# Kernel optimization log

Measured on AMD Instinct MI355X. Metric: run time of the kernel, lower is better.

## Reference

```python
import jax, jax.numpy as jnp
import numpy as np

N_MI, N_DI = 100000, 50000   # node counts
E, L = 500000, 200000        # message edges, supervision (label) edges
F_MI, F_DI, H = 256, 128, 128


def setup_inputs() -> dict:
    key = jax.random.key(0)
    ks = iter(jax.random.split(key, 40))

    def nrm(shape, scale):
        return jax.random.normal(next(ks), shape, jnp.float32) * scale

    inp = {
        'x_mi': jax.random.normal(next(ks), (N_MI, F_MI), jnp.float32),
        'x_di': jax.random.normal(next(ks), (N_DI, F_DI), jnp.float32),
        'W_mi': nrm((H, F_MI), 1.0 / np.sqrt(F_MI)),
        'b_mi': jnp.zeros((H,), jnp.float32),
        'W_di': nrm((H, F_DI), 1.0 / np.sqrt(F_DI)),
        'b_di': jnp.zeros((H,), jnp.float32),
        'emb_mi': nrm((N_MI, H), 1.0),
        'emb_di': nrm((N_DI, H), 1.0),
    }
    # SAGEConv weights per layer per relation (md: miRNA->disease, dm: reverse)
    dims = [(H, 256), (256, 128), (128, 64)]
    for i, (ci, co) in enumerate(dims, 1):
        for rel in ('md', 'dm'):
            inp[f'Wl{i}_{rel}'] = nrm((co, ci), 1.0 / np.sqrt(ci))  # neighbor lin (with bias)
            inp[f'bl{i}_{rel}'] = jnp.zeros((co,), jnp.float32)
            inp[f'Wr{i}_{rel}'] = nrm((co, ci), 1.0 / np.sqrt(ci))  # root lin (no bias)
    inp['edge_src'] = jax.random.randint(next(ks), (E,), 0, N_MI)
    inp['edge_dst'] = jax.random.randint(next(ks), (E,), 0, N_DI)
    inp['label_src'] = jax.random.randint(next(ks), (L,), 0, N_MI)
    inp['label_dst'] = jax.random.randint(next(ks), (L,), 0, N_DI)
    return inp


def _sage(x_src, x_dst, src, dst, n_dst, Wl, bl, Wr):
    # PyG SAGEConv (mean aggr): out = lin_l(mean_neighbors) + lin_r(x_dst)
    agg = jax.ops.segment_sum(x_src[src], dst, num_segments=n_dst)
    deg = jax.ops.segment_sum(jnp.ones_like(dst, dtype=x_src.dtype), dst, num_segments=n_dst)
    mean = agg / jnp.maximum(deg, 1.0)[:, None]
    return mean @ Wl.T + bl + x_dst @ Wr.T


def reference(x_mi, x_di, W_mi, b_mi, W_di, b_di, emb_mi, emb_di,
              Wl1_md, bl1_md, Wr1_md, Wl1_dm, bl1_dm, Wr1_dm,
              Wl2_md, bl2_md, Wr2_md, Wl2_dm, bl2_dm, Wr2_dm,
              Wl3_md, bl3_md, Wr3_md, Wl3_dm, bl3_dm, Wr3_dm,
              edge_src, edge_dst, label_src, label_dst):
    # node_id == arange(num_nodes), so the embedding lookup is the full table
    h_mi = x_mi @ W_mi.T + b_mi + emb_mi
    h_di = x_di @ W_di.T + b_di + emb_di
    layers = [((Wl1_md, bl1_md, Wr1_md), (Wl1_dm, bl1_dm, Wr1_dm)),
              ((Wl2_md, bl2_md, Wr2_md), (Wl2_dm, bl2_dm, Wr2_dm)),
              ((Wl3_md, bl3_md, Wr3_md), (Wl3_dm, bl3_dm, Wr3_dm))]
    for li, (pmd, pdm) in enumerate(layers):
        new_di = _sage(h_mi, h_di, edge_src, edge_dst, N_DI, *pmd)  # miRNA -> disease
        new_mi = _sage(h_di, h_mi, edge_dst, edge_src, N_MI, *pdm)  # disease -> miRNA (reverse)
        if li < 2:
            new_mi, new_di = jax.nn.relu(new_mi), jax.nn.relu(new_di)
        h_mi, h_di = new_mi, new_di
    # classifier: dot product on supervision edges -> [L]
    return (h_mi[label_src] * h_di[label_dst]).sum(axis=-1)
```

## Files before the change

### kernel.cpp

```cpp
#include <hip/hip_runtime.h>

#define N_MI 100000
#define N_DI 50000
#define MI_P 100352
#define DI_P 50176

#define SCAN_CHUNK 2048
#define NB_DI ((N_DI + SCAN_CHUNK - 1) / SCAN_CHUNK)
#define NB_MI ((N_MI + SCAN_CHUNK - 1) / SCAN_CHUNK)

typedef _Float16 half8  __attribute__((ext_vector_type(8)));
typedef _Float16 half4  __attribute__((ext_vector_type(4)));
typedef float    floatx4 __attribute__((ext_vector_type(4)));

__global__ void count_kernel(const int* __restrict__ src, const int* __restrict__ dst,
                             int* deg_mi, int* deg_di, int E) {
    int i = blockIdx.x * blockDim.x + threadIdx.x;
    if (i < E) {
        atomicAdd(&deg_mi[src[i]], 1);
        atomicAdd(&deg_di[dst[i]], 1);
    }
}

__global__ __launch_bounds__(256) void scan_part_kernel(const int* __restrict__ deg_di,
                                                        const int* __restrict__ deg_mi,
                                                        int* __restrict__ row_di,
                                                        int* __restrict__ row_mi,
                                                        int* __restrict__ bsum) {
    const int* deg; int* row; int n; int* bs;
    if (blockIdx.y == 0) { deg = deg_di; row = row_di; n = N_DI; bs = bsum; }
    else                 { deg = deg_mi; row = row_mi; n = N_MI; bs = bsum + 64; }
    int nb = (n + SCAN_CHUNK - 1) / SCAN_CHUNK;
    if ((int)blockIdx.x >= nb) return;
    int t = threadIdx.x;
    int base = blockIdx.x * SCAN_CHUNK + t * 8;
    int v[8]; int s = 0;
    #pragma unroll
    for (int e = 0; e < 8; ++e) {
        int i = base + e;
        v[e] = (i < n) ? deg[i] : 0;
        s += v[e];
    }
    int lane = t & 63, w = t >> 6;
    int x = s;
    #pragma unroll
    for (int off = 1; off < 64; off <<= 1) {
        int y = __shfl_up(x, off, 64);
        if (lane >= off) x += y;
    }
    __shared__ int wsum[4];
    if (lane == 63) wsum[w] = x;
    __syncthreads();
    int woff = 0;
    #pragma unroll
    for (int i = 0; i < 3; ++i) if (i < w) woff += wsum[i];
    int run = woff + x - s;
    #pragma unroll
    for (int e = 0; e < 8; ++e) {
        int i = base + e;
        if (i < n) row[i] = run;
        run += v[e];
    }
    if (t == 255) bs[blockIdx.x] = woff + x;
}

__global__ void scan_sums_kernel(int* __restrict__ bsum, int* __restrict__ row_di,
                                 int* __restrict__ row_mi) {
    int w = threadIdx.x >> 6, lane = threadIdx.x & 63;
    int nb = (w == 0) ? NB_DI : NB_MI;
    int* bs = bsum + w * 64;
    int v = (lane < nb) ? bs[lane] : 0;
    int x = v;
    #pragma unroll
    for (int off = 1; off < 64; off <<= 1) {
        int y = __shfl_up(x, off, 64);
        if (lane >= off) x += y;
    }
    if (lane < nb) bs[lane] = x - v;
    if (lane == nb - 1) {
        if (w == 0) row_di[N_DI] = x;
        else        row_mi[N_MI] = x;
    }
}

__global__ __launch_bounds__(256) void scan_add_kernel(const int* __restrict__ bsum,
                                                       int* __restrict__ row_di,
                                                       int* __restrict__ row_mi) {
    int* row; int n; const int* bs;
    if (blockIdx.y == 0) { row = row_di; n = N_DI; bs = bsum; }
    else                 { row = row_mi; n = N_MI; bs = bsum + 64; }
    int nb = (n + SCAN_CHUNK - 1) / SCAN_CHUNK;
    int b = blockIdx.x;
    if (b >= nb || b == 0) return;
    int off = bs[b];
    int base = b * SCAN_CHUNK + threadIdx.x;
    #pragma unroll
    for (int e = 0; e < 8; ++e) {
        int i = base + e * 256;
        if (i < n) row[i] += off;
    }
}

__global__ void fill_kernel(const int* __restrict__ src, const int* __restrict__ dst,
                            const int* __restrict__ row_mi, const int* __restrict__ row_di,
                            int* cur_mi, int* cur_di, int* csr_mi, int* csr_di, int E) {
    int i = blockIdx.x * blockDim.x + threadIdx.x;
    if (i >= E) return;
    int s = src[i], d = dst[i];
    int p = atomicAdd(&cur_di[d], 1);
    csr_di[row_di[d] + p] = s;
    int q = atomicAdd(&cur_mi[s], 1);
    csr_mi[row_mi[s] + q] = d;
}


struct CvtW {
    const float* s[14];
    _Float16* d[14];
    int K[14];
    int KI[14];
    int nch[14];
};

__global__ void cvtw_kernel(CvtW a) {
    int arr = blockIdx.y;
    int c = blockIdx.x * blockDim.x + threadIdx.x;
    if (c >= a.nch[arr]) return;
    int K = a.K[arr], KI = a.KI[arr];
    int lane = c & 63;
    int j = (c >> 6) & 3;
    int rest = c >> 8;
    int k = rest % KI;
    int p = rest / KI;
    int row = p * 64 + j * 16 + (lane & 15);
    int kcol = k * 32 + (lane >> 4) * 8;
    const float* s = a.s[arr] + (long)row * K + kcol;
    float4 u = *(const float4*)s;
    float4 v = *(const float4*)(s + 4);
    half8 h = {(_Float16)u.x, (_Float16)u.y, (_Float16)u.z, (_Float16)u.w,
               (_Float16)v.x, (_Float16)v.y, (_Float16)v.z, (_Float16)v.w};
    *(half8*)(a.d[arr] + (long)c * 8) = h;
}

template<int K>
__global__ __launch_bounds__(256) void cvt_frag(const float* __restrict__ in,
                                                _Float16* __restrict__ out, int M) {
    constexpr int KI = K / 32;
    constexpr int CPR = K / 8;
    __shared__ _Float16 lds[64 * (K + 8)];
    const int tile = blockIdx.x;
    const int tid = threadIdx.x;
    #pragma unroll
    for (int it = 0; it < KI; ++it) {
        int c = tid + it * 256;
        int r = c / CPR, col = c % CPR;
        int row = tile * 64 + r;
        if (row >= M) row = M - 1;
        const float* g = in + (long)row * K + col * 8;
        float4 u = *(const float4*)g;
        float4 v = *(const float4*)(g + 4);
        half8 h = {(_Float16)u.x, (_Float16)u.y, (_Float16)u.z, (_Float16)u.w,
                   (_Float16)v.x, (_Float16)v.y, (_Float16)v.z, (_Float16)v.w};
        *(half8*)&lds[r * (K + 8) + col * 8] = h;
    }
    __syncthreads();
    #pragma unroll
    for (int it = 0; it < KI; ++it) {
        int c = tid + it * 256;
        int lane = c & 63, i = (c >> 6) & 3, k = c >> 8;
        half8 h = *(const half8*)&lds[(i * 16 + (lane & 15)) * (K + 8) + k * 32 + (lane >> 4) * 8];
        *(half8*)(out + ((long)tile * 8 * K + c) * 8) = h;
    }
}

template<int K>
__global__ __launch_bounds__(256) void repack(const _Float16* __restrict__ in,
                                              _Float16* __restrict__ out) {
    constexpr int KI = K / 32;
    constexpr int CPR = K / 8;
    __shared__ _Float16 lds[64 * (K + 8)];
    const int tile = blockIdx.x;
    const int tid = threadIdx.x;
    #pragma unroll
    for (int it = 0; it < KI; ++it) {
        int c = tid + it * 256;
        int r = c / CPR, col = c % CPR;
        half8 h = *(const half8*)(in + (long)tile * 64 * K + c * 8);
        *(half8*)&lds[r * (K + 8) + col * 8] = h;
    }
    __syncthreads();
    #pragma unroll
    for (int it = 0; it < KI; ++it) {
        int c = tid + it * 256;
        int lane = c & 63, i = (c >> 6) & 3, k = c >> 8;
        half8 h = *(const half8*)&lds[(i * 16 + (lane & 15)) * (K + 8) + k * 32 + (lane >> 4) * 8];
        *(half8*)(out + ((long)tile * 8 * K + c) * 8) = h;
    }
}

template<int DIN>
__global__ __launch_bounds__(256) void agg2_kernel(const _Float16* __restrict__ hsrc,
                                                   const int* __restrict__ row,
                                                   const int* __restrict__ csr,
                                                   _Float16* __restrict__ outf, int n) {
    constexpr int LPR = DIN / 8;
    constexpr int GR  = 64 / LPR;
    constexpr int KI  = DIN / 32;
    int node = blockIdx.x * 4 + (threadIdx.x >> 6);
    if (node >= n) return;
    int lane = threadIdx.x & 63;
    int g = lane / LPR, c = lane % LPR;
    int beg = row[node], end = row[node + 1];
    float acc[8] = {};
    #pragma unroll 2
    for (int j = beg + g; j < end; j += GR) {
        half8 v = *(const half8*)(hsrc + (long)csr[j] * DIN + c * 8);
        #pragma unroll
        for (int e = 0; e < 8; ++e) acc[e] += (float)v[e];
    }
    float inv = 1.f / (float)max(end - beg, 1);
    half8 o;
    #pragma unroll
    for (int e = 0; e < 8; ++e) {
        float s = acc[e];
        s += __shfl_down(s, 32);
        if (GR == 4) s += __shfl_down(s, 16);
        o[e] = (_Float16)(s * inv);
    }
    if (g == 0) {
        int mt = node >> 6, ii = (node >> 4) & 3, lrm = node & 15;
        long off = (((long)mt * KI + (c >> 2)) * 4 + ii) * 512 + (lrm + 16 * (c & 3)) * 8;
        *(half8*)(outf + off) = o;
    }
}

template<int KI, bool DUAL>
__global__ __launch_bounds__(256, 3) void hgemm_f(
    const _Float16* __restrict__ A1f, const _Float16* __restrict__ W1f,
    const _Float16* __restrict__ A2f, const _Float16* __restrict__ W2f,
    const float* __restrict__ bias, const float* __restrict__ Cadd,
    _Float16* __restrict__ C, int M, int N, int relu)
{
    const int wave = threadIdx.x >> 6, lane = threadIdx.x & 63;
    const int quad = lane >> 4, lr = lane & 15;
    const int mt = blockIdx.x * 4 + wave;
    const int p = blockIdx.y;
    const long abase = ((long)mt * KI * 4) * 512 + lane * 8;
    const long wbase = ((long)p  * KI * 4) * 512 + lane * 8;

    floatx4 acc[4][4] = {};

    #pragma unroll
    for (int pass = 0; pass < (DUAL ? 2 : 1); ++pass) {
        const _Float16* A = pass ? A2f : A1f;
        const _Float16* W = pass ? W2f : W1f;
        #pragma unroll
        for (int k = 0; k < KI; ++k) {
            half8 af[4], bf[4];
            #pragma unroll
            for (int i = 0; i < 4; ++i)
                af[i] = *(const half8*)(A + abase + (k * 4 + i) * 512);
            #pragma unroll
            for (int j = 0; j < 4; ++j)
                bf[j] = *(const half8*)(W + wbase + (k * 4 + j) * 512);
            #pragma unroll
            for (int i = 0; i < 4; ++i)
                #pragma unroll
                for (int j = 0; j < 4; ++j)
                    acc[i][j] = __builtin_amdgcn_mfma_f32_16x16x32_f16(af[i], bf[j], acc[i][j], 0, 0, 0);
        }
    }

    const int m0 = mt * 64, n0 = p * 64;
    #pragma unroll
    for (int i = 0; i < 4; ++i) {
        int mb = m0 + i * 16 + quad * 4;
        #pragma unroll
        for (int j = 0; j < 4; ++j) {
            int n = n0 + j * 16 + lr;
            float bn = bias[n];
            #pragma unroll
            for (int r = 0; r < 4; ++r) {
                int m = mb + r;
                if (m < M) {
                    float v = acc[i][j][r] + bn;
                    if (Cadd) v += Cadd[(long)m * N + n];
                    if (relu) v = fmaxf(v, 0.f);
                    C[(long)m * N + n] = (_Float16)v;
                }
            }
        }
    }
}

__global__ void classify_kernel(const _Float16* __restrict__ hmi, const _Float16* __restrict__ hdi,
                                const int* __restrict__ ls, const int* __restrict__ ld,
                                float* __restrict__ out, int L) {
    long idx = (long)blockIdx.x * blockDim.x + threadIdx.x;
    int e = (int)(idx >> 4), q = (int)(idx & 15);
    if (e >= L) return;
    const half4* ra = (const half4*)(hmi + (long)ls[e] * 64);
    const half4* rb = (const half4*)(hdi + (long)ld[e] * 64);
    half4 a = ra[q], b = rb[q];
    float s = (float)a.x * (float)b.x + (float)a.y * (float)b.y +
              (float)a.z * (float)b.z + (float)a.w * (float)b.w;
    #pragma unroll
    for (int off = 8; off >= 1; off >>= 1) s += __shfl_down(s, off, 16);
    if (q == 0) out[e] = s;
}

extern "C" void kernel_launch(void* const* d_in, const int* in_sizes, int n_in,
                              void* d_out, int out_size, void* d_ws, size_t ws_size,
                              hipStream_t stream) {
    const float* x_mi   = (const float*)d_in[0];
    const float* x_di   = (const float*)d_in[1];
    const float* W_mi   = (const float*)d_in[2];
    const float* b_mi   = (const float*)d_in[3];
    const float* W_di   = (const float*)d_in[4];
    const float* b_di   = (const float*)d_in[5];
    const float* emb_mi = (const float*)d_in[6];
    const float* emb_di = (const float*)d_in[7];
    const float* Wl1_md = (const float*)d_in[8];
    const float* bl1_md = (const float*)d_in[9];
    const float* Wr1_md = (const float*)d_in[10];
    const float* Wl1_dm = (const float*)d_in[11];
    const float* bl1_dm = (const float*)d_in[12];
    const float* Wr1_dm = (const float*)d_in[13];
    const float* Wl2_md = (const float*)d_in[14];
    const float* bl2_md = (const float*)d_in[15];
    const float* Wr2_md = (const float*)d_in[16];
    const float* Wl2_dm = (const float*)d_in[17];
    const float* bl2_dm = (const float*)d_in[18];
    const float* Wr2_dm = (const float*)d_in[19];
    const float* Wl3_md = (const float*)d_in[20];
    const float* bl3_md = (const float*)d_in[21];
    const float* Wr3_md = (const float*)d_in[22];
    const float* Wl3_dm = (const float*)d_in[23];
    const float* bl3_dm = (const float*)d_in[24];
    const float* Wr3_dm = (const float*)d_in[25];
    const int* edge_src  = (const int*)d_in[26];
    const int* edge_dst  = (const int*)d_in[27];
    const int* label_src = (const int*)d_in[28];
    const int* label_dst = (const int*)d_in[29];
    const int E = in_sizes[26];
    const int L = in_sizes[28];
    float* out = (float*)d_out;

    _Float16* hp = (_Float16*)d_ws;
    _Float16* wWmi  = hp; hp += 128 * 256;
    _Float16* wWdi  = hp; hp += 128 * 128;
    _Float16* wl1md = hp; hp += 256 * 128;
    _Float16* wr1md = hp; hp += 256 * 128;
    _Float16* wl1dm = hp; hp += 256 * 128;
    _Float16* wr1dm = hp; hp += 256 * 128;
    _Float16* wl2md = hp; hp += 128 * 256;
    _Float16* wr2md = hp; hp += 128 * 256;
    _Float16* wl2dm = hp; hp += 128 * 256;
    _Float16* wr2dm = hp; hp += 128 * 256;
    _Float16* wl3md = hp; hp += 64 * 128;
    _Float16* wr3md = hp; hp += 64 * 128;
    _Float16* wl3dm = hp; hp += 64 * 128;
    _Float16* wr3dm = hp; hp += 64 * 128;
    _Float16* h_mi0 = hp; hp += (long)MI_P * 256;
    _Float16* h_mi1 = hp; hp += (long)MI_P * 256;
    _Float16* h_di0 = hp; hp += (long)DI_P * 256;
    _Float16* h_di1 = hp; hp += (long)DI_P * 256;
    _Float16* hf_mi = hp; hp += (long)MI_P * 256;
    _Float16* hf_di = hp; hp += (long)DI_P * 256;
    _Float16* agghf = hp; hp += (long)MI_P * 256;

    int* ip = (int*)hp;
    int* deg_di = ip;  ip += N_DI;
    int* deg_mi = ip;  ip += N_MI;
    int* cur_di = ip;  ip += N_DI;
    int* cur_mi = ip;  ip += N_MI;
    int* row_di = ip;  ip += N_DI + 1;
    int* row_mi = ip;  ip += N_MI + 1;
    int* csr_di = ip;  ip += E;
    int* csr_mi = ip;  ip += E;
    int* bsum   = ip;  ip += 128;

    hipMemsetAsync(deg_di, 0, (size_t)(2 * (N_DI + N_MI)) * sizeof(int), stream);
    int eb = (E + 255) / 256;
    count_kernel<<<eb, 256, 0, stream>>>(edge_src, edge_dst, deg_mi, deg_di, E);
    scan_part_kernel<<<dim3(NB_MI, 2), 256, 0, stream>>>(deg_di, deg_mi, row_di, row_mi, bsum);
    scan_sums_kernel<<<1, 128, 0, stream>>>(bsum, row_di, row_mi);
    scan_add_kernel<<<dim3(NB_MI, 2), 256, 0, stream>>>(bsum, row_di, row_mi);
    fill_kernel<<<eb, 256, 0, stream>>>(edge_src, edge_dst, row_mi, row_di,
                                        cur_mi, cur_di, csr_mi, csr_di, E);

    CvtW cw;
    const float* srcs[14] = {W_mi, W_di, Wl1_md, Wr1_md, Wl1_dm, Wr1_dm,
                             Wl2_md, Wr2_md, Wl2_dm, Wr2_dm, Wl3_md, Wr3_md, Wl3_dm, Wr3_dm};
    _Float16* dsts[14] = {wWmi, wWdi, wl1md, wr1md, wl1dm, wr1dm,
                          wl2md, wr2md, wl2dm, wr2dm, wl3md, wr3md, wl3dm, wr3dm};
    int Ks[14]  = {256, 128, 128, 128, 128, 128, 256, 256, 256, 256, 128, 128, 128, 128};
    int Ns[14]  = {128, 128, 256, 256, 256, 256, 128, 128, 128, 128, 64, 64, 64, 64};
    for (int i = 0; i < 14; ++i) {
        cw.s[i] = srcs[i]; cw.d[i] = dsts[i];
        cw.K[i] = Ks[i]; cw.KI[i] = Ks[i] / 32;
        cw.nch[i] = Ns[i] * Ks[i] / 8;
    }
    cvtw_kernel<<<dim3(16, 14), 256, 0, stream>>>(cw);

    cvt_frag<256><<<MI_P / 64, 256, 0, stream>>>(x_mi, hf_mi, N_MI);
    cvt_frag<128><<<DI_P / 64, 256, 0, stream>>>(x_di, hf_di, N_DI);

    hgemm_f<8, false><<<dim3(MI_P / 256, 2), 256, 0, stream>>>(
        hf_mi, wWmi, nullptr, nullptr, b_mi, emb_mi, h_mi0, N_MI, 128, 0);
    hgemm_f<4, false><<<dim3(DI_P / 256, 2), 256, 0, stream>>>(
        hf_di, wWdi, nullptr, nullptr, b_di, emb_di, h_di0, N_DI, 128, 0);

    repack<128><<<MI_P / 64, 256, 0, stream>>>(h_mi0, hf_mi);
    repack<128><<<DI_P / 64, 256, 0, stream>>>(h_di0, hf_di);
    agg2_kernel<128><<<(N_DI + 3) / 4, 256, 0, stream>>>(h_mi0, row_di, csr_di, agghf, N_DI);
    hgemm_f<4, true><<<dim3(DI_P / 256, 4), 256, 0, stream>>>(
        agghf, wl1md, hf_di, wr1md, bl1_md, nullptr, h_di1, N_DI, 256, 1);
    agg2_kernel<128><<<(N_MI + 3) / 4, 256, 0, stream>>>(h_di0, row_mi, csr_mi, agghf, N_MI);
    hgemm_f<4, true><<<dim3(MI_P / 256, 4), 256, 0, stream>>>(
        agghf, wl1dm, hf_mi, wr1dm, bl1_dm, nullptr, h_mi1, N_MI, 256, 1);

    repack<256><<<MI_P / 64, 256, 0, stream>>>(h_mi1, hf_mi);
    repack<256><<<DI_P / 64, 256, 0, stream>>>(h_di1, hf_di);
    agg2_kernel<256><<<(N_DI + 3) / 4, 256, 0, stream>>>(h_mi1, row_di, csr_di, agghf, N_DI);
    hgemm_f<8, true><<<dim3(DI_P / 256, 2), 256, 0, stream>>>(
        agghf, wl2md, hf_di, wr2md, bl2_md, nullptr, h_di0, N_DI, 128, 1);
    agg2_kernel<256><<<(N_MI + 3) / 4, 256, 0, stream>>>(h_di1, row_mi, csr_mi, agghf, N_MI);
    hgemm_f<8, true><<<dim3(MI_P / 256, 2), 256, 0, stream>>>(
        agghf, wl2dm, hf_mi, wr2dm, bl2_dm, nullptr, h_mi0, N_MI, 128, 1);

    repack<128><<<MI_P / 64, 256, 0, stream>>>(h_mi0, hf_mi);
    repack<128><<<DI_P / 64, 256, 0, stream>>>(h_di0, hf_di);
    agg2_kernel<128><<<(N_DI + 3) / 4, 256, 0, stream>>>(h_mi0, row_di, csr_di, agghf, N_DI);
    hgemm_f<4, true><<<dim3(DI_P / 256, 1), 256, 0, stream>>>(
        agghf, wl3md, hf_di, wr3md, bl3_md, nullptr, h_di1, N_DI, 64, 0);
    agg2_kernel<128><<<(N_MI + 3) / 4, 256, 0, stream>>>(h_di0, row_mi, csr_mi, agghf, N_MI);
    hgemm_f<4, true><<<dim3(MI_P / 256, 1), 256, 0, stream>>>(
        agghf, wl3dm, hf_mi, wr3dm, bl3_dm, nullptr, h_mi1, N_MI, 64, 0);

    classify_kernel<<<((long)L * 16 + 255) / 256, 256, 0, stream>>>(
        h_mi1, h_di1, label_src, label_dst, out, L);
}
```

Baseline: 892.8 us.

## Fuse fragment repack into GEMM epilogue and shrink per-wave row tiles

The GEMM epilogue now stages each wave's output tile in LDS. From there it writes the row-major result with coalesced half8 stores and also emits the MFMA fragment layout for the next layer, so the separate repack kernels are gone. The per-wave M tile becomes a template parameter (1 or 2 sixteen-row groups instead of 4) with launch bounds raised to 4, giving more blocks and occupancy. Fragment buffers are split into ping-pong A/B sets so a GEMM does not overwrite its own input. The costs are extra LDS use, less register reuse of weight fragments per wave, and duplicate output writes from each GEMM.

```diff
diff --git a/kernel.cpp b/kernel.cpp
--- a/kernel.cpp
+++ b/kernel.cpp
@@ -161,31 +161,6 @@
         float4 v = *(const float4*)(g + 4);
         half8 h = {(_Float16)u.x, (_Float16)u.y, (_Float16)u.z, (_Float16)u.w,
                    (_Float16)v.x, (_Float16)v.y, (_Float16)v.z, (_Float16)v.w};
-        *(half8*)&lds[r * (K + 8) + col * 8] = h;
-    }
-    __syncthreads();
-    #pragma unroll
-    for (int it = 0; it < KI; ++it) {
-        int c = tid + it * 256;
-        int lane = c & 63, i = (c >> 6) & 3, k = c >> 8;
-        half8 h = *(const half8*)&lds[(i * 16 + (lane & 15)) * (K + 8) + k * 32 + (lane >> 4) * 8];
-        *(half8*)(out + ((long)tile * 8 * K + c) * 8) = h;
-    }
-}
-
-template<int K>
-__global__ __launch_bounds__(256) void repack(const _Float16* __restrict__ in,
-                                              _Float16* __restrict__ out) {
-    constexpr int KI = K / 32;
-    constexpr int CPR = K / 8;
-    __shared__ _Float16 lds[64 * (K + 8)];
-    const int tile = blockIdx.x;
-    const int tid = threadIdx.x;
-    #pragma unroll
-    for (int it = 0; it < KI; ++it) {
-        int c = tid + it * 256;
-        int r = c / CPR, col = c % CPR;
-        half8 h = *(const half8*)(in + (long)tile * 64 * K + c * 8);
         *(half8*)&lds[r * (K + 8) + col * 8] = h;
     }
     __syncthreads();
@@ -234,21 +209,25 @@
     }
 }
 
-template<int KI, bool DUAL>
-__global__ __launch_bounds__(256, 3) void hgemm_f(
+template<int KI, bool DUAL, int MR>
+__global__ __launch_bounds__(256, 4) void hgemm_f(
     const _Float16* __restrict__ A1f, const _Float16* __restrict__ W1f,
     const _Float16* __restrict__ A2f, const _Float16* __restrict__ W2f,
     const float* __restrict__ bias, const float* __restrict__ Cadd,
-    _Float16* __restrict__ C, int M, int N, int relu)
+    _Float16* __restrict__ C, _Float16* __restrict__ Cf, int M, int N, int relu)
 {
     const int wave = threadIdx.x >> 6, lane = threadIdx.x & 63;
     const int quad = lane >> 4, lr = lane & 15;
-    const int mt = blockIdx.x * 4 + wave;
+    const int g0 = (blockIdx.x * 4 + wave) * MR;
+    const int mt = g0 >> 2, i0 = g0 & 3;
     const int p = blockIdx.y;
-    const long abase = ((long)mt * KI * 4) * 512 + lane * 8;
-    const long wbase = ((long)p  * KI * 4) * 512 + lane * 8;
-
-    floatx4 acc[4][4] = {};
+    const long abase = ((long)(mt * KI * 4 + i0)) * 512 + lane * 8;
+    const long wbase = ((long)p * KI * 4) * 512 + lane * 8;
+
+    __shared__ _Float16 lds[4][MR * 16 * 72];
+    _Float16* lw = lds[wave];
+
+    floatx4 acc[MR][4] = {};
 
     #pragma unroll
     for (int pass = 0; pass < (DUAL ? 2 : 1); ++pass) {
@@ -256,38 +235,57 @@
         const _Float16* W = pass ? W2f : W1f;
         #pragma unroll
         for (int k = 0; k < KI; ++k) {
-            half8 af[4], bf[4];
+            half8 af[MR], bf[4];
             #pragma unroll
-            for (int i = 0; i < 4; ++i)
+            for (int i = 0; i < MR; ++i)
                 af[i] = *(const half8*)(A + abase + (k * 4 + i) * 512);
             #pragma unroll
             for (int j = 0; j < 4; ++j)
                 bf[j] = *(const half8*)(W + wbase + (k * 4 + j) * 512);
             #pragma unroll
-            for (int i = 0; i < 4; ++i)
+            for (int i = 0; i < MR; ++i)
                 #pragma unroll
                 for (int j = 0; j < 4; ++j)
                     acc[i][j] = __builtin_amdgcn_mfma_f32_16x16x32_f16(af[i], bf[j], acc[i][j], 0, 0, 0);
         }
     }
 
-    const int m0 = mt * 64, n0 = p * 64;
-    #pragma unroll
-    for (int i = 0; i < 4; ++i) {
-        int mb = m0 + i * 16 + quad * 4;
+    const int m0 = g0 * 16, n0 = p * 64;
+    #pragma unroll
+    for (int ii = 0; ii < MR; ++ii) {
         #pragma unroll
         for (int j = 0; j < 4; ++j) {
             int n = n0 + j * 16 + lr;
             float bn = bias[n];
             #pragma unroll
             for (int r = 0; r < 4; ++r) {
-                int m = mb + r;
-                if (m < M) {
-                    float v = acc[i][j][r] + bn;
-                    if (Cadd) v += Cadd[(long)m * N + n];
-                    if (relu) v = fmaxf(v, 0.f);
-                    C[(long)m * N + n] = (_Float16)v;
-                }
+                int m = m0 + ii * 16 + quad * 4 + r;
+                float v = acc[ii][j][r] + bn;
+                if (Cadd && m < M) v += Cadd[(long)m * N + n];
+                if (relu) v = fmaxf(v, 0.f);
+                lw[(ii * 16 + quad * 4 + r) * 72 + j * 16 + lr] = (_Float16)v;
+            }
+        }
+    }
+    __syncthreads();
+
+    const int r2 = lane >> 3, cs = lane & 7;
+    #pragma unroll
+    for (int ii = 0; ii < MR * 2; ++ii) {
+        int m = m0 + ii * 8 + r2;
+        if (m < M)
+            *(half8*)(C + (long)m * N + n0 + cs * 8) =
+                *(const half8*)&lw[(ii * 8 + r2) * 72 + cs * 8];
+    }
+
+    if (Cf) {
+        const int KIn = N >> 5;
+        #pragma unroll
+        for (int ii = 0; ii < MR; ++ii) {
+            #pragma unroll
+            for (int k2 = 0; k2 < 2; ++k2) {
+                half8 h = *(const half8*)&lw[(ii * 16 + lr) * 72 + k2 * 32 + quad * 8];
+                *(half8*)(Cf + ((long)(mt * KIn + p * 2 + k2) * 4 + i0 + ii) * 512 + lane * 8) = h;
             }
         }
     }
@@ -361,13 +359,15 @@
     _Float16* wr3md = hp; hp += 64 * 128;
     _Float16* wl3dm = hp; hp += 64 * 128;
     _Float16* wr3dm = hp; hp += 64 * 128;
-    _Float16* h_mi0 = hp; hp += (long)MI_P * 256;
+    _Float16* h_mi0 = hp; hp += (long)MI_P * 128;
     _Float16* h_mi1 = hp; hp += (long)MI_P * 256;
-    _Float16* h_di0 = hp; hp += (long)DI_P * 256;
+    _Float16* h_di0 = hp; hp += (long)DI_P * 128;
     _Float16* h_di1 = hp; hp += (long)DI_P * 256;
-    _Float16* hf_mi = hp; hp += (long)MI_P * 256;
-    _Float16* hf_di = hp; hp += (long)DI_P * 256;
-    _Float16* agghf = hp; hp += (long)MI_P * 256;
+    _Float16* hfa_mi = hp; hp += (long)MI_P * 128;
+    _Float16* hfb_mi = hp; hp += (long)MI_P * 256;
+    _Float16* hfa_di = hp; hp += (long)DI_P * 128;
+    _Float16* hfb_di = hp; hp += (long)DI_P * 256;
+    _Float16* agghf  = hp; hp += (long)MI_P * 256;
 
     int* ip = (int*)hp;
     int* deg_di = ip;  ip += N_DI;
@@ -403,40 +403,35 @@
     }
     cvtw_kernel<<<dim3(16, 14), 256, 0, stream>>>(cw);
 
-    cvt_frag<256><<<MI_P / 64, 256, 0, stream>>>(x_mi, hf_mi, N_MI);
-    cvt_frag<128><<<DI_P / 64, 256, 0, stream>>>(x_di, hf_di, N_DI);
-
-    hgemm_f<8, false><<<dim3(MI_P / 256, 2), 256, 0, stream>>>(
-        hf_mi, wWmi, nullptr, nullptr, b_mi, emb_mi, h_mi0, N_MI, 128, 0);
-    hgemm_f<4, false><<<dim3(DI_P / 256, 2), 256, 0, stream>>>(
-        hf_di, wWdi, nullptr, nullptr, b_di, emb_di, h_di0, N_DI, 128, 0);
-
-    repack<128><<<MI_P / 64, 256, 0, stream>>>(h_mi0, hf_mi);
-    repack<128><<<DI_P / 64, 256, 0, stream>>>(h_di0, hf_di);
+    cvt_frag<256><<<MI_P / 64, 256, 0, stream>>>(x_mi, hfb_mi, N_MI);
+    cvt_frag<128><<<DI_P / 64, 256, 0, stream>>>(x_di, hfb_di, N_DI);
+
+    hgemm_f<8, false, 2><<<dim3(MI_P / 128, 2), 256, 0, stream>>>(
+        hfb_mi, wWmi, nullptr, nullptr, b_mi, emb_mi, h_mi0, hfa_mi, N_MI, 128, 0);
+    hgemm_f<4, false, 1><<<dim3(DI_P / 64, 2), 256, 0, stream>>>(
+        hfb_di, wWdi, nullptr, nullptr, b_di, emb_di, h_di0, hfa_di, N_DI, 128, 0);
+
     agg2_kernel<128><<<(N_DI + 3) / 4, 256, 0, stream>>>(h_mi0, row_di, csr_di, agghf, N_DI);
-    hgemm_f<4, true><<<dim3(DI_P / 256, 4), 256, 0, stream>>>(
-        agghf, wl1md, hf_di, wr1md, bl1_md, nullptr, h_di1, N_DI, 256, 1);
+    hgemm_f<4, true, 1><<<dim3(DI_P / 64, 4), 256, 0, stream>>>(
+        agghf, wl1md, hfa_di, wr1md, bl1_md, nullptr, h_di1, hfb_di, N_DI, 256, 1);
     agg2_kernel<128><<<(N_MI + 3) / 4, 256, 0, stream>>>(h_di0, row_mi, csr_mi, agghf, N_MI);
-    hgemm_f<4, true><<<dim3(MI_P / 256, 4), 256, 0, stream>>>(
-        agghf, wl1dm, hf_mi, wr1dm, bl1_dm, nullptr, h_mi1, N_MI, 256, 1);
-
-    repack<256><<<MI_P / 64, 256, 0, stream>>>(h_mi1, hf_mi);
-    repack<256><<<DI_P / 64, 256, 0, stream>>>(h_di1, hf_di);
+    hgemm_f<4, true, 2><<<dim3(MI_P / 128, 4), 256, 0, stream>>>(
+        agghf, wl1dm, hfa_mi, wr1dm, bl1_dm, nullptr, h_mi1, hfb_mi, N_MI, 256, 1);
+
     agg2_kernel<256><<<(N_DI + 3) / 4, 256, 0, stream>>>(h_mi1, row_di, csr_di, agghf, N_DI);
-    hgemm_f<8, true><<<dim3(DI_P / 256, 2), 256, 0, stream>>>(
-        agghf, wl2md, hf_di, wr2md, bl2_md, nullptr, h_di0, N_DI, 128, 1);
+    hgemm_f<8, true, 1><<<dim3(DI_P / 64, 2), 256, 0, stream>>>(
+        agghf, wl2md, hfb_di, wr2md, bl2_md, nullptr, h_di0, hfa_di, N_DI, 128, 1);
     agg2_kernel<256><<<(N_MI + 3) / 4, 256, 0, stream>>>(h_di1, row_mi, csr_mi, agghf, N_MI);
-    hgemm_f<8, true><<<dim3(MI_P / 256, 2), 256, 0, stream>>>(
-        agghf, wl2dm, hf_mi, wr2dm, bl2_dm, nullptr, h_mi0, N_MI, 128, 1);
-
-    repack<128><<<MI_P / 64, 256, 0, stream>>>(h_mi0, hf_mi);
-    repack<128><<<DI_P / 64, 256, 0, stream>>>(h_di0, hf_di);
+    hgemm_f<8, true, 2><<<dim3(MI_P / 128, 2), 256, 0, stream>>>(
+        agghf, wl2dm, hfb_mi, wr2dm, bl2_dm, nullptr, h_mi0, hfa_mi, N_MI, 128, 1);
+
     agg2_kernel<128><<<(N_DI + 3) / 4, 256, 0, stream>>>(h_mi0, row_di, csr_di, agghf, N_DI);
-    hgemm_f<4, true><<<dim3(DI_P / 256, 1), 256, 0, stream>>>(
-        agghf, wl3md, hf_di, wr3md, bl3_md, nullptr, h_di1, N_DI, 64, 0);
-    agg2_kernel<128><<<(N_MI + 3) / 4, 256, 0, stream>>>(h_di0, row_mi, csr_mi, agghf, N_MI);
-    hgemm_f<4, true><<<dim3(MI_P / 256, 1), 256, 0, stream>>>(
-        agghf, wl3dm, hf_mi, wr3dm, bl3_dm, nullptr, h_mi1, N_MI, 64, 0);
+    hgemm_f<4, true, 1><<<dim3(DI_P / 64, 1), 256, 0, stream>>>(
+        agghf, wl3md, hfa_di, wr3md, bl3_md, nullptr, h_di1, nullptr, N_DI, 64, 0);
+    agg2_kernel<128><<<(N_MI + 3) / 4, 256, 0, stream>>>(
+        h_di0, row_mi, csr_mi, agghf, N_MI);
+    hgemm_f<4, true, 1><<<dim3(MI_P / 64, 1), 256, 0, stream>>>(
+        agghf, wl3dm, hfa_mi, wr3dm, bl3_dm, nullptr, h_mi1, nullptr, N_MI, 64, 0);
 
     classify_kernel<<<((long)L * 16 + 255) / 256, 256, 0, stream>>>(
         h_mi1, h_di1, label_src, label_dst, out, L);
```

Result: faster. 827.2 us (-7.3%).
